# Performance work log

Hardware: AMD Instinct MI355X
Metric: run time of the kernel (lower is better)

## Reference

```python
import jax, jax.numpy as jnp
import numpy as np

NEG_INF = -100000000.0  # matches masked_fill value in torch source

def setup_inputs() -> dict:
    key = jax.random.key(0)
    ks = jax.random.split(key, 7)
    d_model, d = 1024, 128
    B, S = 4, 2048
    scale = 1.0 / np.sqrt(d_model)
    x = jax.random.normal(ks[0], (B, S, d_model), dtype=jnp.float32)
    Wq = jax.random.normal(ks[1], (d, d_model), dtype=jnp.float32) * scale
    bq = jax.random.normal(ks[2], (d,), dtype=jnp.float32) * 0.02
    Wk = jax.random.normal(ks[3], (d, d_model), dtype=jnp.float32) * scale
    bk = jax.random.normal(ks[4], (d,), dtype=jnp.float32) * 0.02
    Wv = jax.random.normal(ks[5], (d, d_model), dtype=jnp.float32) * scale
    bv = jax.random.normal(ks[6], (d,), dtype=jnp.float32) * 0.02
    return {"x": x, "Wq": Wq, "bq": bq, "Wk": Wk, "bk": bk, "Wv": Wv, "bv": bv}

def reference(x, Wq, bq, Wk, bk, Wv, bv):
    # Q,K,V: [B,S,d] via torch Linear (x @ W.T + b)
    Q = jnp.einsum('bsm,dm->bsd', x, Wq) + bq
    K = jnp.einsum('bsm,dm->bsd', x, Wk) + bk
    V = jnp.einsum('bsm,dm->bsd', x, Wv) + bv
    d = Wk.shape[0]
    scale = 1.0 / jnp.sqrt(jnp.asarray(d, dtype=Q.dtype))
    scores = jnp.einsum('bqd,bkd->bqk', Q, K) * scale  # [B,S,S]
    # Faithful to source: tril then value-based mask (tril==0 -> -1e8).
    tril = jnp.tril(scores)
    masked = jnp.where(tril == 0, NEG_INF, tril)
    attn = jax.nn.softmax(masked, axis=-1)
    context = jnp.einsum('bqk,bkd->bqd', attn, V)
    return context
```

## Files before the change

kernel.cpp:

```cpp
#include <hip/hip_runtime.h>

typedef __attribute__((ext_vector_type(8))) short bf16x8;
typedef __attribute__((ext_vector_type(4))) float f32x4;

__device__ __forceinline__ unsigned short f2bf(float f) {
    unsigned int u = __float_as_uint(f);
    u += 0x7fffu + ((u >> 16) & 1u);
    return (unsigned short)(u >> 16);
}
__device__ __forceinline__ unsigned int pack2bf(float lo, float hi) {
    return (unsigned int)f2bf(lo) | ((unsigned int)f2bf(hi) << 16);
}
__device__ __forceinline__ void async_ld16(void* lds, const void* g) {
    __builtin_amdgcn_global_load_lds(
        (const __attribute__((address_space(1))) unsigned int*)g,
        (__attribute__((address_space(3))) unsigned int*)lds, 16, 0, 0);
}

__global__ __launch_bounds__(256) void convert_bf16(
    const float* __restrict__ x,
    const float* __restrict__ Wq, const float* __restrict__ Wk,
    const float* __restrict__ Wv,
    unsigned short* __restrict__ xbf, unsigned short* __restrict__ Wcat)
{
    const size_t XN8 = (size_t)8192 * 1024 / 8;
    size_t i = (size_t)blockIdx.x * 256 + threadIdx.x;
    const float* src;
    unsigned short* dst;
    if (i < XN8) {
        src = x + i * 8;
        dst = xbf + i * 8;
    } else {
        size_t o = (i - XN8) * 8;
        int sel = (int)(o >> 17);
        const float* W = (sel == 0) ? Wq : ((sel == 1) ? Wk : Wv);
        src = W + (o & 131071);
        dst = Wcat + o;
    }
    float4 f0 = ((const float4*)src)[0];
    float4 f1 = ((const float4*)src)[1];
    uint4 u;
    u.x = pack2bf(f0.x, f0.y); u.y = pack2bf(f0.z, f0.w);
    u.z = pack2bf(f1.x, f1.y); u.w = pack2bf(f1.z, f1.w);
    *(uint4*)dst = u;
}

__global__ __launch_bounds__(256) void qkv_gemm(
    const unsigned short* __restrict__ xbf,
    const unsigned short* __restrict__ Wcat,
    const float* __restrict__ bq, const float* __restrict__ bk,
    const float* __restrict__ bv,
    unsigned short* __restrict__ Qg,
    unsigned short* __restrict__ Kg,
    unsigned short* __restrict__ Vtg)
{
    __shared__ unsigned short As[2][32 * 64];
    __shared__ unsigned short Bs[2][128 * 64];

    const int tid  = threadIdx.x;
    const int lane = tid & 63;
    const int w    = tid >> 6;
    const int quad = lane >> 4;
    const int ln   = lane & 15;
    const int lr   = lane >> 3;
    const int csw  = ((lane & 7) ^ lr) * 8;

    const int bid   = blockIdx.x;
    const int mbase = (bid / 3) * 32;
    const int nb    = bid % 3;
    const unsigned short* Wsel = Wcat + (size_t)nb * 128 * 1024;

    f32x4 acc[2][2];
#pragma unroll
    for (int mt = 0; mt < 2; mt++)
#pragma unroll
        for (int nt = 0; nt < 2; nt++) acc[mt][nt] = (f32x4){0.f, 0.f, 0.f, 0.f};

    auto stage = [&](int kb, int p) {
        const int kcol = kb * 64 + csw;
        async_ld16(&As[p][w * 512 + lane * 8],
                   xbf + (size_t)(mbase + w * 8 + lr) * 1024 + kcol);
#pragma unroll
        for (int j = 0; j < 4; j++) {
            int chunk = w * 4 + j;
            async_ld16(&Bs[p][chunk * 512 + lane * 8],
                       Wsel + (size_t)(chunk * 8 + lr) * 1024 + kcol);
        }
    };

    stage(0, 0);
    __syncthreads();

    for (int kb = 0; kb < 16; kb++) {
        const int p = kb & 1;
        if (kb < 15) stage(kb + 1, p ^ 1);
#pragma unroll
        for (int ks = 0; ks < 2; ks++) {
            bf16x8 a[2], b[2];
#pragma unroll
            for (int mt = 0; mt < 2; mt++) {
                int row = mt * 16 + ln;
                a[mt] = *(const bf16x8*)&As[p][row * 64 + ((ks * 4 + quad) ^ (ln & 7)) * 8];
            }
#pragma unroll
            for (int nt = 0; nt < 2; nt++) {
                int row = w * 32 + nt * 16 + ln;
                b[nt] = *(const bf16x8*)&Bs[p][row * 64 + ((ks * 4 + quad) ^ (ln & 7)) * 8];
            }
#pragma unroll
            for (int mt = 0; mt < 2; mt++)
#pragma unroll
                for (int nt = 0; nt < 2; nt++)
                    acc[mt][nt] = __builtin_amdgcn_mfma_f32_16x16x32_bf16(
                        a[mt], b[nt], acc[mt][nt], 0, 0, 0);
        }
        __syncthreads();
    }

    const float scale = (nb == 0) ? 0.08838834764831845f : 1.0f;
    const float* bsel = (nb == 0) ? bq : ((nb == 1) ? bk : bv);
    float bias_v[2];
#pragma unroll
    for (int nt = 0; nt < 2; nt++) bias_v[nt] = bsel[w * 32 + nt * 16 + ln];

    if (nb < 2) {
        unsigned short* dst = (nb == 0) ? Qg : Kg;
#pragma unroll
        for (int mt = 0; mt < 2; mt++)
#pragma unroll
            for (int nt = 0; nt < 2; nt++)
#pragma unroll
                for (int r = 0; r < 4; r++) {
                    int m = mbase + mt * 16 + quad * 4 + r;
                    int d = w * 32 + nt * 16 + ln;
                    dst[(size_t)m * 128 + d] =
                        f2bf((acc[mt][nt][r] + bias_v[nt]) * scale);
                }
    } else {
#pragma unroll
        for (int mt = 0; mt < 2; mt++)
#pragma unroll
            for (int nt = 0; nt < 2; nt++) {
                int dd = w * 32 + nt * 16 + ln;
                int m0 = mbase + mt * 16 + quad * 4;
                int bb = m0 >> 11, s0 = m0 & 2047;
                ushort4 u = { f2bf(acc[mt][nt][0] + bias_v[nt]),
                              f2bf(acc[mt][nt][1] + bias_v[nt]),
                              f2bf(acc[mt][nt][2] + bias_v[nt]),
                              f2bf(acc[mt][nt][3] + bias_v[nt]) };
                *(ushort4*)&Vtg[((size_t)bb * 128 + dd) * 2048 + s0] = u;
            }
    }
}

__global__ __launch_bounds__(256) void flash_attn(
    const unsigned short* __restrict__ Qg,
    const unsigned short* __restrict__ Kg,
    const unsigned short* __restrict__ Vtg,
    unsigned short* __restrict__ Opart,
    float2* __restrict__ ml)
{
    __shared__ unsigned short Ks[2][64 * 128];
    __shared__ unsigned short Vts[2][128 * 64];
    __shared__ unsigned short Pl[64][72];

    const int b = blockIdx.x;
    const int q = blockIdx.y;
    const int c = blockIdx.z;
    if (c > (q >> 2)) return;

    const int m4 = q >> 2, r4 = q & 3;
    const int pidx = b * 144 + q + 2 * m4 * (m4 - 1) + r4 * m4 + c;
    const int k0 = c * 4;
    const int kend = (c * 4 + 4 < q + 1) ? (c * 4 + 4) : (q + 1);

    const int tid  = threadIdx.x;
    const int lane = tid & 63, w = tid >> 6, quad = lane >> 4, ln = lane & 15;

    bf16x8 qa[4];
    const unsigned short* qrow =
        Qg + ((size_t)b * 2048 + q * 64 + w * 16 + ln) * 128 + quad * 8;
#pragma unroll
    for (int ks = 0; ks < 4; ks++) qa[ks] = *(const bf16x8*)(qrow + ks * 32);

    auto stage = [&](int kt, int p) {
        const unsigned short* ksrc = Kg + ((size_t)b * 2048 + kt * 64) * 128;
        const int krl = lane >> 4;
#pragma unroll
        for (int j = 0; j < 4; j++) {
            int chunk = w * 4 + j;
            int row = chunk * 4 + krl;
            int cd = (lane & 15) ^ (row & 15);
            async_ld16(&Ks[p][chunk * 512 + lane * 8],
                       ksrc + (size_t)row * 128 + cd * 8);
        }
        const unsigned short* vsrc = Vtg + (size_t)b * 128 * 2048 + kt * 64;
        const int vrl = lane >> 3;
#pragma unroll
        for (int j = 0; j < 4; j++) {
            int chunk = w * 4 + j;
            int row = chunk * 8 + vrl;
            int cd = (lane & 7) ^ (row & 7);
            async_ld16(&Vts[p][chunk * 512 + lane * 8],
                       vsrc + (size_t)row * 2048 + cd * 8);
        }
    };

    float m_i[4], l_i[4];
    f32x4 Ofr[8];
#pragma unroll
    for (int r = 0; r < 4; r++) { m_i[r] = -__builtin_inff(); l_i[r] = 0.f; }
#pragma unroll
    for (int dt = 0; dt < 8; dt++) Ofr[dt] = (f32x4){0.f, 0.f, 0.f, 0.f};

    stage(k0, 0);
    __syncthreads();

    int p = 0;
    for (int kt = k0; kt < kend; kt++) {
        if (kt + 1 < kend) stage(kt + 1, p ^ 1);

        f32x4 sfr[4];
#pragma unroll
        for (int ct = 0; ct < 4; ct++) {
            f32x4 s = (f32x4){0.f, 0.f, 0.f, 0.f};
#pragma unroll
            for (int ks = 0; ks < 4; ks++) {
                int row = ct * 16 + ln;
                bf16x8 kf = *(const bf16x8*)&Ks[p][row * 128 + ((ks * 4 + quad) ^ ln) * 8];
                s = __builtin_amdgcn_mfma_f32_16x16x32_bf16(qa[ks], kf, s, 0, 0, 0);
            }
            sfr[ct] = s;
        }

        if (kt == q) {
#pragma unroll
            for (int ct = 0; ct < 4; ct++)
#pragma unroll
                for (int r = 0; r < 4; r++)
                    if (ct * 16 + ln > w * 16 + quad * 4 + r)
                        sfr[ct][r] = -__builtin_inff();
        }

        float mrow[4];
#pragma unroll
        for (int r = 0; r < 4; r++) mrow[r] = -__builtin_inff();
#pragma unroll
        for (int ct = 0; ct < 4; ct++)
#pragma unroll
            for (int r = 0; r < 4; r++) mrow[r] = fmaxf(mrow[r], sfr[ct][r]);
#pragma unroll
        for (int off = 1; off < 16; off <<= 1)
#pragma unroll
            for (int r = 0; r < 4; r++)
                mrow[r] = fmaxf(mrow[r], __shfl_xor(mrow[r], off, 64));

        float alpha[4], rs[4];
#pragma unroll
        for (int r = 0; r < 4; r++) {
            float mn = fmaxf(m_i[r], mrow[r]);
            alpha[r] = __expf(m_i[r] - mn);
            m_i[r]   = mn;
            rs[r]    = 0.f;
        }
#pragma unroll
        for (int ct = 0; ct < 4; ct++)
#pragma unroll
            for (int r = 0; r < 4; r++) {
                float pv = __expf(sfr[ct][r] - m_i[r]);
                rs[r] += pv;
                Pl[w * 16 + quad * 4 + r][ct * 16 + ln] = f2bf(pv);
            }
#pragma unroll
        for (int off = 1; off < 16; off <<= 1)
#pragma unroll
            for (int r = 0; r < 4; r++) rs[r] += __shfl_xor(rs[r], off, 64);
#pragma unroll
        for (int r = 0; r < 4; r++) l_i[r] = l_i[r] * alpha[r] + rs[r];
#pragma unroll
        for (int dt = 0; dt < 8; dt++)
#pragma unroll
            for (int r = 0; r < 4; r++) Ofr[dt][r] *= alpha[r];

        __syncthreads();

#pragma unroll
        for (int kstep = 0; kstep < 2; kstep++) {
            bf16x8 pa = *(const bf16x8*)&Pl[w * 16 + ln][kstep * 32 + quad * 8];
#pragma unroll
            for (int dt = 0; dt < 8; dt++) {
                int row = dt * 16 + ln;
                bf16x8 vf = *(const bf16x8*)&Vts[p][row * 64 + ((kstep * 4 + quad) ^ (ln & 7)) * 8];
                Ofr[dt] = __builtin_amdgcn_mfma_f32_16x16x32_bf16(pa, vf, Ofr[dt], 0, 0, 0);
            }
        }
        __syncthreads();
        p ^= 1;
    }

#pragma unroll
    for (int dt = 0; dt < 8; dt++)
#pragma unroll
        for (int r = 0; r < 4; r++) {
            int row = w * 16 + quad * 4 + r;
            Opart[((size_t)pidx * 64 + row) * 128 + dt * 16 + ln] = f2bf(Ofr[dt][r]);
        }
    if (ln == 0) {
#pragma unroll
        for (int r = 0; r < 4; r++) {
            int row = w * 16 + quad * 4 + r;
            ml[(size_t)pidx * 64 + row] = make_float2(m_i[r], l_i[r]);
        }
    }
}

__global__ __launch_bounds__(256) void combine(
    const unsigned short* __restrict__ Opart,
    const float2* __restrict__ ml,
    float* __restrict__ out)
{
    const int b = blockIdx.x >> 5, q = blockIdx.x & 31;
    const int m4 = q >> 2, r4 = q & 3;
    const int pbase = b * 144 + q + 2 * m4 * (m4 - 1) + r4 * m4;
    const int nc = m4 + 1;

    const int row = threadIdx.x & 63;
    const int grp = (threadIdx.x >> 6) * 32;

    float2 t[8];
#pragma unroll
    for (int c2 = 0; c2 < 8; c2++) {
        int cc = (c2 < nc) ? c2 : (nc - 1);
        t[c2] = ml[(size_t)(pbase + cc) * 64 + row];
    }
    float mc[8], lc[8], wgt[8];
    float mmax = -__builtin_inff();
#pragma unroll
    for (int c2 = 0; c2 < 8; c2++) {
        mc[c2] = (c2 < nc) ? t[c2].x : -__builtin_inff();
        lc[c2] = (c2 < nc) ? t[c2].y : 0.f;
        mmax = fmaxf(mmax, mc[c2]);
    }
    float lsum = 0.f;
#pragma unroll
    for (int c2 = 0; c2 < 8; c2++) {
        wgt[c2] = __expf(mc[c2] - mmax);
        lsum += lc[c2] * wgt[c2];
    }
    const float inv = 1.0f / lsum;

#pragma unroll
    for (int v = 0; v < 4; v++) {
        int col = grp + v * 8;
        float acc[8];
#pragma unroll
        for (int k = 0; k < 8; k++) acc[k] = 0.f;
#pragma unroll
        for (int c2 = 0; c2 < 8; c2++) {
            int cc = (c2 < nc) ? c2 : (nc - 1);
            uint4 u = *(const uint4*)&Opart[((size_t)(pbase + cc) * 64 + row) * 128 + col];
            float wc = wgt[c2];
            acc[0] += wc * __uint_as_float(u.x << 16);
            acc[1] += wc * __uint_as_float(u.x & 0xffff0000u);
            acc[2] += wc * __uint_as_float(u.y << 16);
            acc[3] += wc * __uint_as_float(u.y & 0xffff0000u);
            acc[4] += wc * __uint_as_float(u.z << 16);
            acc[5] += wc * __uint_as_float(u.z & 0xffff0000u);
            acc[6] += wc * __uint_as_float(u.w << 16);
            acc[7] += wc * __uint_as_float(u.w & 0xffff0000u);
        }
        float* o = &out[((size_t)b * 2048 + q * 64 + row) * 128 + col];
        float4 o0 = { acc[0] * inv, acc[1] * inv, acc[2] * inv, acc[3] * inv };
        float4 o1 = { acc[4] * inv, acc[5] * inv, acc[6] * inv, acc[7] * inv };
        ((float4*)o)[0] = o0;
        ((float4*)o)[1] = o1;
    }
}

extern "C" void kernel_launch(void* const* d_in, const int* in_sizes, int n_in,
                              void* d_out, int out_size, void* d_ws, size_t ws_size,
                              hipStream_t stream) {
    const float* x  = (const float*)d_in[0];
    const float* Wq = (const float*)d_in[1];
    const float* bq = (const float*)d_in[2];
    const float* Wk = (const float*)d_in[3];
    const float* bk = (const float*)d_in[4];
    const float* Wv = (const float*)d_in[5];
    const float* bv = (const float*)d_in[6];
    float* out = (float*)d_out;

    char* wsb = (char*)d_ws;
    unsigned short* xbf   = (unsigned short*)wsb;
    unsigned short* Wcat  = (unsigned short*)(wsb + 16777216);
    unsigned short* Opart = (unsigned short*)wsb;
    float2*         ml    = (float2*)(wsb + 9437184);
    unsigned short* Qg    = (unsigned short*)(wsb + 17563648);
    unsigned short* Kg    = Qg + (size_t)8192 * 128;
    unsigned short* Vtg   = Qg + (size_t)2 * 8192 * 128;

    convert_bf16<<<4288, 256, 0, stream>>>(x, Wq, Wk, Wv, xbf, Wcat);
    qkv_gemm<<<768, 256, 0, stream>>>(xbf, Wcat, bq, bk, bv, Qg, Kg, Vtg);
    flash_attn<<<dim3(4, 32, 8), 256, 0, stream>>>(Qg, Kg, Vtg, Opart, ml);
    combine<<<128, 256, 0, stream>>>(Opart, ml, out);
}
```

Measured before the change: 139.1 us.

## Fuse x bf16 conversion into QKV GEMM A-tile loads and split combine blocks

The separate pass that converted x to bf16 is removed. The QKV GEMM now loads fp32 x through registers, converts it in-kernel and writes swizzled bf16 into LDS, overlapping the next tile's load with the MFMAs. Only the weights are still pre-converted. Block order is changed so blocks sharing the same weight slice run together, and the combine kernel is split into twice as many blocks, each covering half the columns. This saves a 32MB round trip through global memory, at the cost of each x tile being read and converted three times (once per Q/K/V block) and of extra register pressure.

```diff
diff --git a/kernel.cpp b/kernel.cpp
--- a/kernel.cpp
+++ b/kernel.cpp
@@ -17,36 +17,24 @@
         (__attribute__((address_space(3))) unsigned int*)lds, 16, 0, 0);
 }
 
-__global__ __launch_bounds__(256) void convert_bf16(
-    const float* __restrict__ x,
+__global__ __launch_bounds__(256) void conv_w(
     const float* __restrict__ Wq, const float* __restrict__ Wk,
-    const float* __restrict__ Wv,
-    unsigned short* __restrict__ xbf, unsigned short* __restrict__ Wcat)
+    const float* __restrict__ Wv, unsigned short* __restrict__ Wcat)
 {
-    const size_t XN8 = (size_t)8192 * 1024 / 8;
-    size_t i = (size_t)blockIdx.x * 256 + threadIdx.x;
-    const float* src;
-    unsigned short* dst;
-    if (i < XN8) {
-        src = x + i * 8;
-        dst = xbf + i * 8;
-    } else {
-        size_t o = (i - XN8) * 8;
-        int sel = (int)(o >> 17);
-        const float* W = (sel == 0) ? Wq : ((sel == 1) ? Wk : Wv);
-        src = W + (o & 131071);
-        dst = Wcat + o;
-    }
+    size_t o = ((size_t)blockIdx.x * 256 + threadIdx.x) * 8;
+    int sel = (int)(o >> 17);
+    const float* W = (sel == 0) ? Wq : ((sel == 1) ? Wk : Wv);
+    const float* src = W + (o & 131071);
     float4 f0 = ((const float4*)src)[0];
     float4 f1 = ((const float4*)src)[1];
     uint4 u;
     u.x = pack2bf(f0.x, f0.y); u.y = pack2bf(f0.z, f0.w);
     u.z = pack2bf(f1.x, f1.y); u.w = pack2bf(f1.z, f1.w);
-    *(uint4*)dst = u;
+    *(uint4*)(Wcat + o) = u;
 }
 
 __global__ __launch_bounds__(256) void qkv_gemm(
-    const unsigned short* __restrict__ xbf,
+    const float* __restrict__ x,
     const unsigned short* __restrict__ Wcat,
     const float* __restrict__ bq, const float* __restrict__ bk,
     const float* __restrict__ bv,
@@ -66,20 +54,25 @@
     const int csw  = ((lane & 7) ^ lr) * 8;
 
     const int bid   = blockIdx.x;
-    const int mbase = (bid / 3) * 32;
-    const int nb    = bid % 3;
+    const int nb    = bid >> 8;
+    const int mbase = (bid & 255) * 32;
     const unsigned short* Wsel = Wcat + (size_t)nb * 128 * 1024;
 
+    const int arow  = tid >> 3;
+    const int achk  = tid & 7;
+    const int aslot = achk ^ (arow & 7);
+    const float* xsrc = x + (size_t)(mbase + arow) * 1024 + achk * 8;
+    unsigned short* adst0 = &As[0][arow * 64 + aslot * 8];
+    unsigned short* adst1 = &As[1][arow * 64 + aslot * 8];
+
     f32x4 acc[2][2];
 #pragma unroll
     for (int mt = 0; mt < 2; mt++)
 #pragma unroll
         for (int nt = 0; nt < 2; nt++) acc[mt][nt] = (f32x4){0.f, 0.f, 0.f, 0.f};
 
-    auto stage = [&](int kb, int p) {
+    auto stageB = [&](int kb, int p) {
         const int kcol = kb * 64 + csw;
-        async_ld16(&As[p][w * 512 + lane * 8],
-                   xbf + (size_t)(mbase + w * 8 + lr) * 1024 + kcol);
 #pragma unroll
         for (int j = 0; j < 4; j++) {
             int chunk = w * 4 + j;
@@ -87,13 +80,28 @@
                        Wsel + (size_t)(chunk * 8 + lr) * 1024 + kcol);
         }
     };
-
-    stage(0, 0);
+    auto writeA = [&](int p, const float4& f0, const float4& f1) {
+        uint4 u;
+        u.x = pack2bf(f0.x, f0.y); u.y = pack2bf(f0.z, f0.w);
+        u.z = pack2bf(f1.x, f1.y); u.w = pack2bf(f1.z, f1.w);
+        *(uint4*)((p == 0) ? adst0 : adst1) = u;
+    };
+
+    float4 a0 = ((const float4*)xsrc)[0];
+    float4 a1 = ((const float4*)xsrc)[1];
+    stageB(0, 0);
+    writeA(0, a0, a1);
     __syncthreads();
 
     for (int kb = 0; kb < 16; kb++) {
         const int p = kb & 1;
-        if (kb < 15) stage(kb + 1, p ^ 1);
+        float4 n0, n1;
+        if (kb < 15) {
+            stageB(kb + 1, p ^ 1);
+            const float* xs = xsrc + (kb + 1) * 64;
+            n0 = ((const float4*)xs)[0];
+            n1 = ((const float4*)xs)[1];
+        }
 #pragma unroll
         for (int ks = 0; ks < 2; ks++) {
             bf16x8 a[2], b[2];
@@ -114,6 +122,7 @@
                     acc[mt][nt] = __builtin_amdgcn_mfma_f32_16x16x32_bf16(
                         a[mt], b[nt], acc[mt][nt], 0, 0, 0);
         }
+        if (kb < 15) writeA(p ^ 1, n0, n1);
         __syncthreads();
     }
 
@@ -319,13 +328,15 @@
     const float2* __restrict__ ml,
     float* __restrict__ out)
 {
-    const int b = blockIdx.x >> 5, q = blockIdx.x & 31;
+    const int idx  = blockIdx.x >> 1;
+    const int half = blockIdx.x & 1;
+    const int b = idx >> 5, q = idx & 31;
     const int m4 = q >> 2, r4 = q & 3;
     const int pbase = b * 144 + q + 2 * m4 * (m4 - 1) + r4 * m4;
     const int nc = m4 + 1;
 
     const int row = threadIdx.x & 63;
-    const int grp = (threadIdx.x >> 6) * 32;
+    const int grp = half * 64 + (threadIdx.x >> 6) * 16;
 
     float2 t[8];
 #pragma unroll
@@ -350,7 +361,7 @@
     const float inv = 1.0f / lsum;
 
 #pragma unroll
-    for (int v = 0; v < 4; v++) {
+    for (int v = 0; v < 2; v++) {
         int col = grp + v * 8;
         float acc[8];
 #pragma unroll
@@ -390,16 +401,15 @@
     float* out = (float*)d_out;
 
     char* wsb = (char*)d_ws;
-    unsigned short* xbf   = (unsigned short*)wsb;
-    unsigned short* Wcat  = (unsigned short*)(wsb + 16777216);
     unsigned short* Opart = (unsigned short*)wsb;
     float2*         ml    = (float2*)(wsb + 9437184);
-    unsigned short* Qg    = (unsigned short*)(wsb + 17563648);
+    unsigned short* Wcat  = (unsigned short*)(wsb + 10485760);
+    unsigned short* Qg    = (unsigned short*)(wsb + 11272192);
     unsigned short* Kg    = Qg + (size_t)8192 * 128;
     unsigned short* Vtg   = Qg + (size_t)2 * 8192 * 128;
 
-    convert_bf16<<<4288, 256, 0, stream>>>(x, Wq, Wk, Wv, xbf, Wcat);
-    qkv_gemm<<<768, 256, 0, stream>>>(xbf, Wcat, bq, bk, bv, Qg, Kg, Vtg);
+    conv_w<<<192, 256, 0, stream>>>(Wq, Wk, Wv, Wcat);
+    qkv_gemm<<<768, 256, 0, stream>>>(x, Wcat, bq, bk, bv, Qg, Kg, Vtg);
     flash_attn<<<dim3(4, 32, 8), 256, 0, stream>>>(Qg, Kg, Vtg, Opart, ml);
-    combine<<<128, 256, 0, stream>>>(Opart, ml, out);
-}
+    combine<<<256, 256, 0, stream>>>(Opart, ml, out);
+}
```

Result: faster. 129.1 us (-7.2%).
